# Performance work log

Measured on AMD Instinct MI355X. Metric: run time of the kernel, lower is better.

The kernel has to match this reference:

```python
import jax, jax.numpy as jnp
import numpy as np

B, S, D, H = 2, 2048, 1024, 16
HD = D // H  # head_dim = 64


def setup_inputs() -> dict:
    key = jax.random.key(0)
    ks = jax.random.split(key, 6)
    scale = 1.0 / np.sqrt(D)
    return {
        "x": jax.random.normal(ks[0], (B, S, D), dtype=jnp.float32),
        "Wq": jax.random.normal(ks[1], (D, D), dtype=jnp.float32) * scale,
        "bq": jnp.zeros((D,), dtype=jnp.float32),
        "Wk": jax.random.normal(ks[2], (D, D), dtype=jnp.float32) * scale,
        "bk": jnp.zeros((D,), dtype=jnp.float32),
        "Wv": jax.random.normal(ks[3], (D, D), dtype=jnp.float32) * scale,
        "bv": jnp.zeros((D,), dtype=jnp.float32),
        "Wo": jax.random.normal(ks[4], (D, D), dtype=jnp.float32) * scale,
        "bo": jnp.zeros((D,), dtype=jnp.float32),
    }


def reference(x, Wq, bq, Wk, bk, Wv, bv, Wo, bo):
    b, s, d = x.shape
    # q/k/v projections; torch Linear computes x @ W.T + b (W here stored as [out,in])
    q = (x @ Wq.T + bq).reshape(b, s, H, HD).transpose(0, 2, 1, 3)  # [b,h,s,hd]
    k = (x @ Wk.T + bk).reshape(b, s, H, HD).transpose(0, 2, 1, 3)
    v = (x @ Wv.T + bv).reshape(b, s, H, HD).transpose(0, 2, 1, 3)
    scores = jnp.einsum("bhqd,bhkd->bhqk", q, k) / jnp.sqrt(jnp.float32(HD))
    attn = jax.nn.softmax(scores, axis=-1)  # dropout p=0.0 -> identity
    ctx = jnp.einsum("bhqk,bhkd->bhqd", attn, v)
    ctx = ctx.transpose(0, 2, 1, 3).reshape(b, s, d)
    out = ctx @ Wo.T + bo
    return out, attn
```

## Files before the change

### kernel.cpp

```cpp
#include <hip/hip_runtime.h>
#include <hip/hip_bf16.h>


typedef __attribute__((ext_vector_type(8))) __bf16 bf16x8;
typedef __attribute__((ext_vector_type(8))) short short8;
typedef __attribute__((ext_vector_type(4))) float f32x4;
typedef __attribute__((ext_vector_type(4))) float float4v;
typedef __attribute__((ext_vector_type(4))) unsigned short ushort4v;
typedef __attribute__((ext_vector_type(8))) unsigned short ushort8v;

#define DEV static __device__ __forceinline__

DEV unsigned short f2bf(float f) {
  unsigned int u = __builtin_bit_cast(unsigned int, f);
  u += 0x7FFFu + ((u >> 16) & 1u);
  return (unsigned short)(u >> 16);
}

DEV float exp2v(float x) {
#if __has_builtin(__builtin_amdgcn_exp2f)
  return __builtin_amdgcn_exp2f(x);
#else
  return exp2f(x);
#endif
}

DEV f32x4 mfma16(short8 a, short8 b, f32x4 c) {
  return __builtin_amdgcn_mfma_f32_16x16x32_bf16(
      __builtin_bit_cast(bf16x8, a), __builtin_bit_cast(bf16x8, b), c, 0, 0, 0);
}

DEV void gld16(const void* g, void* l) {
  __builtin_amdgcn_global_load_lds(
      (const __attribute__((address_space(1))) void*)g,
      (__attribute__((address_space(3))) void*)l, 16, 0, 0);
}

#define QSCALE 0.18033688011112042f

__global__ __launch_bounds__(256) void cvt_all(
    const float* __restrict__ x, const float* __restrict__ wq,
    const float* __restrict__ wk, const float* __restrict__ wv,
    const float* __restrict__ wo, unsigned short* __restrict__ xb,
    unsigned short* __restrict__ wqb, unsigned short* __restrict__ wkb,
    unsigned short* __restrict__ wvb, unsigned short* __restrict__ wob) {
  const int bid = blockIdx.x;
  const float* s;
  unsigned short* d;
  int base;
  if (bid < 2048) {
    s = x; d = xb; base = bid * 2048;
  } else {
    const int j = bid - 2048, sel = j >> 9;
    s = sel == 0 ? wq : (sel == 1 ? wk : (sel == 2 ? wv : wo));
    d = sel == 0 ? wqb : (sel == 1 ? wkb : (sel == 2 ? wvb : wob));
    base = (j & 511) * 2048;
  }
  const int i = base + threadIdx.x * 8;
  float4v v0 = *(const float4v*)(s + i);
  float4v v1 = *(const float4v*)(s + i + 4);
  ushort8v o = {f2bf(v0[0]), f2bf(v0[1]), f2bf(v0[2]), f2bf(v0[3]),
                f2bf(v1[0]), f2bf(v1[1]), f2bf(v1[2]), f2bf(v1[3])};
  *(ushort8v*)(d + i) = o;
}

template <int WBF>
__global__ __launch_bounds__(256, 3) void gemm_qkv(
    const unsigned short* __restrict__ xb,
    const void* __restrict__ W0, const void* __restrict__ W1, const void* __restrict__ W2,
    const float* __restrict__ b0, const float* __restrict__ b1, const float* __restrict__ b2,
    unsigned short* __restrict__ Qw, unsigned short* __restrict__ Kw,
    unsigned short* __restrict__ Vt) {
  constexpr int K = 1024;
  __shared__ unsigned short As[2][128 * 32];
  __shared__ unsigned short Bs[2][128 * 32];
  const int tid = threadIdx.x, lane = tid & 63, w = tid >> 6;
  const int g = lane >> 4, ln = lane & 15;
  const int wm = (w >> 1) * 64, wn = (w & 1) * 64;
  const int work = ((int)blockIdx.x & 7) * 96 + ((int)blockIdx.x >> 3);
  const int t = work >> 8, tn = (work >> 5) & 7, tm = work & 31;
  const int m0 = tm * 128, n0 = tn * 128;
  const void* Wsel = t == 0 ? W0 : (t == 1 ? W1 : W2);
  const float* bsel = t == 0 ? b0 : (t == 1 ? b1 : b2);
  const float osc = t == 0 ? QSCALE : 1.0f;

  const unsigned short* Abase = xb + (size_t)(m0 + (tid >> 2)) * K + (tid & 3) * 8;
  const unsigned short* Bb16 = (const unsigned short*)Wsel + (size_t)(n0 + (tid >> 2)) * K + (tid & 3) * 8;
  const float* Bf32 = (const float*)Wsel + (size_t)(n0 + (tid >> 1)) * K + (tid & 1) * 16;
  const int bwoff = (tid >> 1) * 32 + (tid & 1) * 16;

  f32x4 acc[4][4] = {};

  gld16(Abase, &As[0][tid * 8]);
  gld16(Abase + (size_t)64 * K, &As[0][2048 + tid * 8]);
  if (WBF) {
    gld16(Bb16, &Bs[0][tid * 8]);
    gld16(Bb16 + (size_t)64 * K, &Bs[0][2048 + tid * 8]);
  } else {
    float4v u0 = *(const float4v*)Bf32, u1 = *(const float4v*)(Bf32 + 4);
    float4v u2 = *(const float4v*)(Bf32 + 8), u3 = *(const float4v*)(Bf32 + 12);
    ushort8v o0 = {f2bf(u0[0]), f2bf(u0[1]), f2bf(u0[2]), f2bf(u0[3]),
                   f2bf(u1[0]), f2bf(u1[1]), f2bf(u1[2]), f2bf(u1[3])};
    ushort8v o1 = {f2bf(u2[0]), f2bf(u2[1]), f2bf(u2[2]), f2bf(u2[3]),
                   f2bf(u3[0]), f2bf(u3[1]), f2bf(u3[2]), f2bf(u3[3])};
    *(ushort8v*)&Bs[0][bwoff] = o0;
    *(ushort8v*)&Bs[0][bwoff + 8] = o1;
  }

#pragma unroll 2
  for (int it = 0; it < 32; ++it) {
    __syncthreads();
    const int cur = it & 1, nxt = cur ^ 1;
    float4v u0, u1, u2, u3;
    if (it + 1 < 32) {
      const int k1 = (it + 1) * 32;
      gld16(Abase + k1, &As[nxt][tid * 8]);
      gld16(Abase + (size_t)64 * K + k1, &As[nxt][2048 + tid * 8]);
      if (WBF) {
        gld16(Bb16 + k1, &Bs[nxt][tid * 8]);
        gld16(Bb16 + (size_t)64 * K + k1, &Bs[nxt][2048 + tid * 8]);
      } else {
        u0 = *(const float4v*)(Bf32 + k1);
        u1 = *(const float4v*)(Bf32 + k1 + 4);
        u2 = *(const float4v*)(Bf32 + k1 + 8);
        u3 = *(const float4v*)(Bf32 + k1 + 12);
      }
    }
    short8 a[4], bfr[4];
#pragma unroll
    for (int fi = 0; fi < 4; ++fi)
      a[fi] = *(const short8*)&As[cur][(wm + fi * 16 + ln) * 32 + g * 8];
#pragma unroll
    for (int fj = 0; fj < 4; ++fj)
      bfr[fj] = *(const short8*)&Bs[cur][(wn + fj * 16 + ln) * 32 + g * 8];
#pragma unroll
    for (int fi = 0; fi < 4; ++fi)
#pragma unroll
      for (int fj = 0; fj < 4; ++fj) acc[fi][fj] = mfma16(a[fi], bfr[fj], acc[fi][fj]);
    if (!WBF && it + 1 < 32) {
      ushort8v o0 = {f2bf(u0[0]), f2bf(u0[1]), f2bf(u0[2]), f2bf(u0[3]),
                     f2bf(u1[0]), f2bf(u1[1]), f2bf(u1[2]), f2bf(u1[3])};
      ushort8v o1 = {f2bf(u2[0]), f2bf(u2[1]), f2bf(u2[2]), f2bf(u2[3]),
                     f2bf(u3[0]), f2bf(u3[1]), f2bf(u3[2]), f2bf(u3[3])};
      *(ushort8v*)&Bs[nxt][bwoff] = o0;
      *(ushort8v*)&Bs[nxt][bwoff + 8] = o1;
    }
  }

  if (t < 2) {
    unsigned short* Op = t == 0 ? Qw : Kw;
#pragma unroll
    for (int fi = 0; fi < 4; ++fi)
#pragma unroll
      for (int fj = 0; fj < 4; ++fj) {
        const int n = n0 + wn + fj * 16 + ln;
        const float bs = bsel[n];
#pragma unroll
        for (int rr = 0; rr < 4; ++rr) {
          const int m = m0 + wm + fi * 16 + 4 * g + rr;
          Op[(size_t)m * 1024 + n] = f2bf((acc[fi][fj][rr] + bs) * osc);
        }
      }
  } else {
    const int bb = m0 >> 11;
    const int s0 = (m0 & 2047) + wm;
#pragma unroll
    for (int fi = 0; fi < 4; ++fi)
#pragma unroll
      for (int fj = 0; fj < 4; ++fj) {
        const int n = n0 + wn + fj * 16 + ln;
        const float bs = bsel[n];
        ushort4v o = {f2bf(acc[fi][fj][0] + bs), f2bf(acc[fi][fj][1] + bs),
                      f2bf(acc[fi][fj][2] + bs), f2bf(acc[fi][fj][3] + bs)};
        *(ushort4v*)&Vt[(size_t)(bb * 1024 + n) * 2048 + s0 + fi * 16 + 4 * g] = o;
      }
  }
}

template <int WBF>
__global__ __launch_bounds__(256, 3) void gemm_o(const unsigned short* __restrict__ Cw,
                                                 const void* __restrict__ Wo,
                                                 const float* __restrict__ bo,
                                                 float* __restrict__ outp) {
  constexpr int K = 1024;
  __shared__ unsigned short As[2][128 * 32];
  __shared__ unsigned short Bs[2][128 * 32];
  const int tid = threadIdx.x, lane = tid & 63, w = tid >> 6;
  const int g = lane >> 4, ln = lane & 15;
  const int wm = (w >> 1) * 64, wn = (w & 1) * 64;
  const int work = ((int)blockIdx.x & 7) * 32 + ((int)blockIdx.x >> 3);
  const int m0 = (work & 31) * 128, n0 = (work >> 5) * 128;

  const unsigned short* Abase = Cw + (size_t)(m0 + (tid >> 2)) * K + (tid & 3) * 8;
  const unsigned short* Bb16 = (const unsigned short*)Wo + (size_t)(n0 + (tid >> 2)) * K + (tid & 3) * 8;
  const float* Bf32 = (const float*)Wo + (size_t)(n0 + (tid >> 1)) * K + (tid & 1) * 16;
  const int bwoff = (tid >> 1) * 32 + (tid & 1) * 16;

  f32x4 acc[4][4] = {};

  gld16(Abase, &As[0][tid * 8]);
  gld16(Abase + (size_t)64 * K, &As[0][2048 + tid * 8]);
  if (WBF) {
    gld16(Bb16, &Bs[0][tid * 8]);
    gld16(Bb16 + (size_t)64 * K, &Bs[0][2048 + tid * 8]);
  } else {
    float4v u0 = *(const float4v*)Bf32, u1 = *(const float4v*)(Bf32 + 4);
    float4v u2 = *(const float4v*)(Bf32 + 8), u3 = *(const float4v*)(Bf32 + 12);
    ushort8v o0 = {f2bf(u0[0]), f2bf(u0[1]), f2bf(u0[2]), f2bf(u0[3]),
                   f2bf(u1[0]), f2bf(u1[1]), f2bf(u1[2]), f2bf(u1[3])};
    ushort8v o1 = {f2bf(u2[0]), f2bf(u2[1]), f2bf(u2[2]), f2bf(u2[3]),
                   f2bf(u3[0]), f2bf(u3[1]), f2bf(u3[2]), f2bf(u3[3])};
    *(ushort8v*)&Bs[0][bwoff] = o0;
    *(ushort8v*)&Bs[0][bwoff + 8] = o1;
  }

#pragma unroll 2
  for (int it = 0; it < 32; ++it) {
    __syncthreads();
    const int cur = it & 1, nxt = cur ^ 1;
    float4v u0, u1, u2, u3;
    if (it + 1 < 32) {
      const int k1 = (it + 1) * 32;
      gld16(Abase + k1, &As[nxt][tid * 8]);
      gld16(Abase + (size_t)64 * K + k1, &As[nxt][2048 + tid * 8]);
      if (WBF) {
        gld16(Bb16 + k1, &Bs[nxt][tid * 8]);
        gld16(Bb16 + (size_t)64 * K + k1, &Bs[nxt][2048 + tid * 8]);
      } else {
        u0 = *(const float4v*)(Bf32 + k1);
        u1 = *(const float4v*)(Bf32 + k1 + 4);
        u2 = *(const float4v*)(Bf32 + k1 + 8);
        u3 = *(const float4v*)(Bf32 + k1 + 12);
      }
    }
    short8 a[4], bfr[4];
#pragma unroll
    for (int fi = 0; fi < 4; ++fi)
      a[fi] = *(const short8*)&As[cur][(wm + fi * 16 + ln) * 32 + g * 8];
#pragma unroll
    for (int fj = 0; fj < 4; ++fj)
      bfr[fj] = *(const short8*)&Bs[cur][(wn + fj * 16 + ln) * 32 + g * 8];
#pragma unroll
    for (int fi = 0; fi < 4; ++fi)
#pragma unroll
      for (int fj = 0; fj < 4; ++fj) acc[fi][fj] = mfma16(a[fi], bfr[fj], acc[fi][fj]);
    if (!WBF && it + 1 < 32) {
      ushort8v o0 = {f2bf(u0[0]), f2bf(u0[1]), f2bf(u0[2]), f2bf(u0[3]),
                     f2bf(u1[0]), f2bf(u1[1]), f2bf(u1[2]), f2bf(u1[3])};
      ushort8v o1 = {f2bf(u2[0]), f2bf(u2[1]), f2bf(u2[2]), f2bf(u2[3]),
                     f2bf(u3[0]), f2bf(u3[1]), f2bf(u3[2]), f2bf(u3[3])};
      *(ushort8v*)&Bs[nxt][bwoff] = o0;
      *(ushort8v*)&Bs[nxt][bwoff + 8] = o1;
    }
  }

#pragma unroll
  for (int fi = 0; fi < 4; ++fi)
#pragma unroll
    for (int fj = 0; fj < 4; ++fj) {
      const int n = n0 + wn + fj * 16 + ln;
      const float bs = bo[n];
#pragma unroll
      for (int rr = 0; rr < 4; ++rr) {
        const int m = m0 + wm + fi * 16 + 4 * g + rr;
        outp[(size_t)m * 1024 + n] = acc[fi][fj][rr] + bs;
      }
    }
}

__global__ __launch_bounds__(512, 4) void attn_kernel(
    const unsigned short* __restrict__ Qg, const unsigned short* __restrict__ Kg,
    const unsigned short* __restrict__ Vt, float* __restrict__ attn_out,
    unsigned short* __restrict__ ctx) {
  constexpr int LDP = 72;
  __shared__ unsigned short Ps[128 * LDP];
  __shared__ unsigned short Ks[2][64 * 64];
  __shared__ unsigned short Vs[2][64 * 64];
  const int tid = threadIdx.x, lane = tid & 63, w = tid >> 6;
  const int g = lane >> 4, ln = lane & 15;
  const int work = ((int)blockIdx.x & 7) * 64 + ((int)blockIdx.x >> 3);
  const int qt = work & 15, h = (work >> 4) & 15, b = work >> 8;
  const int q0 = qt * 128;
  const size_t kbase = (size_t)b * 2048 * 1024 + (size_t)h * 64;
  const size_t vbase = ((size_t)b * 1024 + h * 64) * 2048;

  short8 qf[2];
#pragma unroll
  for (int hh = 0; hh < 2; ++hh)
    qf[hh] = *(const short8*)(Qg + kbase + (size_t)(q0 + w * 16 + ln) * 1024 +
                              hh * 32 + 8 * g);

  const int sr = tid >> 3, sb = tid & 7;
  const int swz = ((sb ^ (sr & 7)) * 8);
  const unsigned short* Ksrc = Kg + kbase + (size_t)sr * 1024 + swz;
  const unsigned short* Vsrc = Vt + vbase + (size_t)sr * 2048 + swz;

  float lp = 0.f;
  gld16(Ksrc, &Ks[0][tid * 8]);
#pragma unroll 2
  for (int kc = 0; kc < 32; ++kc) {
    __syncthreads();
    if (kc + 1 < 32)
      gld16(Ksrc + (size_t)(kc + 1) * 64 * 1024, &Ks[(kc + 1) & 1][tid * 8]);
    const unsigned short* Kc = Ks[kc & 1];
#pragma unroll
    for (int fk = 0; fk < 4; ++fk) {
      const int row = fk * 16 + ln;
      const short8 kf0 = *(const short8*)&Kc[row * 64 + ((g ^ (ln & 7)) * 8)];
      const short8 kf1 = *(const short8*)&Kc[row * 64 + (((4 + g) ^ (ln & 7)) * 8)];
      f32x4 z = {0.f, 0.f, 0.f, 0.f};
      __builtin_amdgcn_s_setprio(1);
      z = mfma16(kf0, qf[0], z);
      z = mfma16(kf1, qf[1], z);
      __builtin_amdgcn_s_setprio(0);
      lp += exp2v(z[0]) + exp2v(z[1]) + exp2v(z[2]) + exp2v(z[3]);
    }
  }
  lp += __shfl_xor(lp, 16);
  lp += __shfl_xor(lp, 32);
  const float lb = -log2f(lp);

  __syncthreads();
  gld16(Ksrc, &Ks[0][tid * 8]);
  gld16(Vsrc, &Vs[0][tid * 8]);
  f32x4 c_[4] = {};
  const size_t attnbase = ((size_t)(b * 16 + h) * 2048 + q0 + w * 16) * 2048;
#pragma unroll 2
  for (int kc = 0; kc < 32; ++kc) {
    __syncthreads();
    if (kc + 1 < 32) {
      gld16(Ksrc + (size_t)(kc + 1) * 64 * 1024, &Ks[(kc + 1) & 1][tid * 8]);
      gld16(Vsrc + (kc + 1) * 64, &Vs[(kc + 1) & 1][tid * 8]);
    }
    const unsigned short* Kc = Ks[kc & 1];
    const unsigned short* Vc = Vs[kc & 1];
#pragma unroll
    for (int fk = 0; fk < 4; ++fk) {
      const int row = fk * 16 + ln;
      const short8 kf0 = *(const short8*)&Kc[row * 64 + ((g ^ (ln & 7)) * 8)];
      const short8 kf1 = *(const short8*)&Kc[row * 64 + (((4 + g) ^ (ln & 7)) * 8)];
      f32x4 z = {lb, lb, lb, lb};
      __builtin_amdgcn_s_setprio(1);
      z = mfma16(kf0, qf[0], z);
      z = mfma16(kf1, qf[1], z);
      __builtin_amdgcn_s_setprio(0);
      float4v pv = {exp2v(z[0]), exp2v(z[1]), exp2v(z[2]), exp2v(z[3])};
      *(float4v*)&attn_out[attnbase + (size_t)ln * 2048 + kc * 64 + fk * 16 + 4 * g] = pv;
      ushort4v pb = {f2bf(pv[0]), f2bf(pv[1]), f2bf(pv[2]), f2bf(pv[3])};
      *(ushort4v*)&Ps[(w * 16 + ln) * LDP + fk * 16 + 4 * g] = pb;
    }
#pragma unroll
    for (int ks = 0; ks < 2; ++ks) {
      const short8 pa = *(const short8*)&Ps[(w * 16 + ln) * LDP + ks * 32 + 8 * g];
      __builtin_amdgcn_s_setprio(1);
#pragma unroll
      for (int fd = 0; fd < 4; ++fd) {
        const int d = fd * 16 + ln;
        const short8 vb = *(const short8*)&Vc[d * 64 + (((ks * 4 + g) ^ (ln & 7)) * 8)];
        c_[fd] = mfma16(pa, vb, c_[fd]);
      }
      __builtin_amdgcn_s_setprio(0);
    }
  }

#pragma unroll
  for (int fd = 0; fd < 4; ++fd)
#pragma unroll
    for (int rr = 0; rr < 4; ++rr) {
      const int q = w * 16 + 4 * g + rr;
      ctx[(size_t)(b * 2048 + q0 + q) * 1024 + h * 64 + fd * 16 + ln] = f2bf(c_[fd][rr]);
    }
}

extern "C" void kernel_launch(void* const* d_in, const int* in_sizes, int n_in,
                              void* d_out, int out_size, void* d_ws, size_t ws_size,
                              hipStream_t stream) {
  const float* x  = (const float*)d_in[0];
  const float* Wq = (const float*)d_in[1];
  const float* bq = (const float*)d_in[2];
  const float* Wk = (const float*)d_in[3];
  const float* bk = (const float*)d_in[4];
  const float* Wv = (const float*)d_in[5];
  const float* bv = (const float*)d_in[6];
  const float* Wo = (const float*)d_in[7];
  const float* bo = (const float*)d_in[8];

  float* outp = (float*)d_out;
  float* attnp = outp + (size_t)4194304;

  unsigned short* Qw = (unsigned short*)d_ws;
  unsigned short* Kw = Qw + (size_t)4194304;
  unsigned short* Vt = Kw + (size_t)4194304;
  unsigned short* Cw = Vt + (size_t)4194304;

  const bool wbf = ws_size >= (size_t)40 * 1024 * 1024;
  dim3 blk(256, 1, 1);

  if (wbf) {
    unsigned short* Wqb = Cw + (size_t)4194304;
    unsigned short* Wkb = Wqb + (size_t)1048576;
    unsigned short* Wvb = Wkb + (size_t)1048576;
    unsigned short* Wob = Wvb + (size_t)1048576;
    cvt_all<<<dim3(4096), blk, 0, stream>>>(x, Wq, Wk, Wv, Wo, Cw, Wqb, Wkb, Wvb, Wob);
    gemm_qkv<1><<<dim3(768), blk, 0, stream>>>(Cw, Wqb, Wkb, Wvb, bq, bk, bv, Qw, Kw, Vt);
    attn_kernel<<<dim3(512), dim3(512), 0, stream>>>(Qw, Kw, Vt, attnp, Cw);
    gemm_o<1><<<dim3(256), blk, 0, stream>>>(Cw, Wob, bo, outp);
  } else {
    cvt_all<<<dim3(2048), blk, 0, stream>>>(x, Wq, Wk, Wv, Wo, Cw, nullptr, nullptr,
                                            nullptr, nullptr);
    gemm_qkv<0><<<dim3(768), blk, 0, stream>>>(Cw, Wq, Wk, Wv, bq, bk, bv, Qw, Kw, Vt);
    attn_kernel<<<dim3(512), dim3(512), 0, stream>>>(Qw, Kw, Vt, attnp, Cw);
    gemm_o<0><<<dim3(256), blk, 0, stream>>>(Cw, Wo, bo, outp);
  }
}
```

Baseline: 245.1 us.

## Triple-buffer K/V tiles in attention with prefetch distance two and explicit vmcnt waits

```diff
diff --git a/kernel.cpp b/kernel.cpp
--- a/kernel.cpp
+++ b/kernel.cpp
@@ -274,8 +274,8 @@
     unsigned short* __restrict__ ctx) {
   constexpr int LDP = 72;
   __shared__ unsigned short Ps[128 * LDP];
-  __shared__ unsigned short Ks[2][64 * 64];
-  __shared__ unsigned short Vs[2][64 * 64];
+  __shared__ unsigned short Ks[3][64 * 64];
+  __shared__ unsigned short Vs[3][64 * 64];
   const int tid = threadIdx.x, lane = tid & 63, w = tid >> 6;
   const int g = lane >> 4, ln = lane & 15;
   const int work = ((int)blockIdx.x & 7) * 64 + ((int)blockIdx.x >> 3);
@@ -297,12 +297,18 @@
 
   float lp = 0.f;
   gld16(Ksrc, &Ks[0][tid * 8]);
-#pragma unroll 2
+  gld16(Ksrc + (size_t)64 * 1024, &Ks[1][tid * 8]);
   for (int kc = 0; kc < 32; ++kc) {
-    __syncthreads();
-    if (kc + 1 < 32)
-      gld16(Ksrc + (size_t)(kc + 1) * 64 * 1024, &Ks[(kc + 1) & 1][tid * 8]);
-    const unsigned short* Kc = Ks[kc & 1];
+    if (kc < 31)
+      asm volatile("s_waitcnt vmcnt(1)" ::: "memory");
+    else
+      asm volatile("s_waitcnt vmcnt(0)" ::: "memory");
+    __builtin_amdgcn_s_barrier();
+    __builtin_amdgcn_sched_barrier(0);
+    if (kc + 2 < 32)
+      gld16(Ksrc + (size_t)(kc + 2) * 64 * 1024, &Ks[(kc + 2) % 3][tid * 8]);
+    __builtin_amdgcn_sched_barrier(0);
+    const unsigned short* Kc = Ks[kc % 3];
 #pragma unroll
     for (int fk = 0; fk < 4; ++fk) {
       const int row = fk * 16 + ln;
@@ -321,19 +327,29 @@
   const float lb = -log2f(lp);
 
   __syncthreads();
+
   gld16(Ksrc, &Ks[0][tid * 8]);
   gld16(Vsrc, &Vs[0][tid * 8]);
+  gld16(Ksrc + (size_t)64 * 1024, &Ks[1][tid * 8]);
+  gld16(Vsrc + 64, &Vs[1][tid * 8]);
   f32x4 c_[4] = {};
   const size_t attnbase = ((size_t)(b * 16 + h) * 2048 + q0 + w * 16) * 2048;
-#pragma unroll 2
   for (int kc = 0; kc < 32; ++kc) {
-    __syncthreads();
-    if (kc + 1 < 32) {
-      gld16(Ksrc + (size_t)(kc + 1) * 64 * 1024, &Ks[(kc + 1) & 1][tid * 8]);
-      gld16(Vsrc + (kc + 1) * 64, &Vs[(kc + 1) & 1][tid * 8]);
-    }
-    const unsigned short* Kc = Ks[kc & 1];
-    const unsigned short* Vc = Vs[kc & 1];
+    if (kc == 0)
+      asm volatile("s_waitcnt vmcnt(2)" ::: "memory");
+    else if (kc == 1)
+      asm volatile("s_waitcnt vmcnt(6)" ::: "memory");
+    else
+      asm volatile("s_waitcnt vmcnt(8)" ::: "memory");
+    __builtin_amdgcn_s_barrier();
+    __builtin_amdgcn_sched_barrier(0);
+    if (kc + 2 < 32) {
+      gld16(Ksrc + (size_t)(kc + 2) * 64 * 1024, &Ks[(kc + 2) % 3][tid * 8]);
+      gld16(Vsrc + (kc + 2) * 64, &Vs[(kc + 2) % 3][tid * 8]);
+    }
+    __builtin_amdgcn_sched_barrier(0);
+    const unsigned short* Kc = Ks[kc % 3];
+    const unsigned short* Vc = Vs[kc % 3];
 #pragma unroll
     for (int fk = 0; fk < 4; ++fk) {
       const int row = fk * 16 + ln;
```

New measurement: 244.8 us. Within noise of the previous version (-0.1%).

## Split attention row-sum pass into separate kernel parallelised over key halves

Applied to the files above, without the earlier changes.

```diff
diff --git a/kernel.cpp b/kernel.cpp
--- a/kernel.cpp
+++ b/kernel.cpp
@@ -268,10 +268,60 @@
     }
 }
 
-__global__ __launch_bounds__(512, 4) void attn_kernel(
+__global__ __launch_bounds__(512, 6) void attn_pass1(
     const unsigned short* __restrict__ Qg, const unsigned short* __restrict__ Kg,
-    const unsigned short* __restrict__ Vt, float* __restrict__ attn_out,
-    unsigned short* __restrict__ ctx) {
+    float* __restrict__ lpart) {
+  __shared__ unsigned short Ks[2][64 * 64];
+  const int tid = threadIdx.x, lane = tid & 63, w = tid >> 6;
+  const int g = lane >> 4, ln = lane & 15;
+  const int work = ((int)blockIdx.x & 7) * 128 + ((int)blockIdx.x >> 3);
+  const int qt = work & 15, h = (work >> 4) & 15, b = (work >> 8) & 1, kh = work >> 9;
+  const int q0 = qt * 128;
+  const size_t kbase = (size_t)b * 2048 * 1024 + (size_t)h * 64;
+
+  short8 qf[2];
+#pragma unroll
+  for (int hh = 0; hh < 2; ++hh)
+    qf[hh] = *(const short8*)(Qg + kbase + (size_t)(q0 + w * 16 + ln) * 1024 +
+                              hh * 32 + 8 * g);
+
+  const int sr = tid >> 3, sb = tid & 7;
+  const int swz = ((sb ^ (sr & 7)) * 8);
+  const unsigned short* Ksrc = Kg + kbase + (size_t)(kh * 1024 + sr) * 1024 + swz;
+
+  float lp = 0.f;
+  gld16(Ksrc, &Ks[0][tid * 8]);
+#pragma unroll 2
+  for (int kc = 0; kc < 16; ++kc) {
+    __syncthreads();
+    if (kc + 1 < 16)
+      gld16(Ksrc + (size_t)(kc + 1) * 64 * 1024, &Ks[(kc + 1) & 1][tid * 8]);
+    const unsigned short* Kc = Ks[kc & 1];
+#pragma unroll
+    for (int fk = 0; fk < 4; ++fk) {
+      const int row = fk * 16 + ln;
+      const short8 kf0 = *(const short8*)&Kc[row * 64 + ((g ^ (ln & 7)) * 8)];
+      const short8 kf1 = *(const short8*)&Kc[row * 64 + (((4 + g) ^ (ln & 7)) * 8)];
+      f32x4 z = {0.f, 0.f, 0.f, 0.f};
+      __builtin_amdgcn_s_setprio(1);
+      z = mfma16(kf0, qf[0], z);
+      z = mfma16(kf1, qf[1], z);
+      __builtin_amdgcn_s_setprio(0);
+      lp += exp2v(z[0]) + exp2v(z[1]) + exp2v(z[2]) + exp2v(z[3]);
+    }
+  }
+  lp += __shfl_xor(lp, 16);
+  lp += __shfl_xor(lp, 32);
+  if (g == 0 && lane < 16) {
+    const size_t q = (size_t)(b * 16 + h) * 2048 + q0 + w * 16 + ln;
+    lpart[(q << 1) + kh] = lp;
+  }
+}
+
+__global__ __launch_bounds__(512, 4) void attn_pass2(
+    const unsigned short* __restrict__ Qg, const unsigned short* __restrict__ Kg,
+    const unsigned short* __restrict__ Vt, const float* __restrict__ lpart,
+    float* __restrict__ attn_out, unsigned short* __restrict__ ctx) {
   constexpr int LDP = 72;
   __shared__ unsigned short Ps[128 * LDP];
   __shared__ unsigned short Ks[2][64 * 64];
@@ -290,37 +340,14 @@
     qf[hh] = *(const short8*)(Qg + kbase + (size_t)(q0 + w * 16 + ln) * 1024 +
                               hh * 32 + 8 * g);
 
+  const size_t qidx = (size_t)(b * 16 + h) * 2048 + q0 + w * 16 + ln;
+  const float lb = -log2f(lpart[qidx << 1] + lpart[(qidx << 1) + 1]);
+
   const int sr = tid >> 3, sb = tid & 7;
   const int swz = ((sb ^ (sr & 7)) * 8);
   const unsigned short* Ksrc = Kg + kbase + (size_t)sr * 1024 + swz;
   const unsigned short* Vsrc = Vt + vbase + (size_t)sr * 2048 + swz;
 
-  float lp = 0.f;
-  gld16(Ksrc, &Ks[0][tid * 8]);
-#pragma unroll 2
-  for (int kc = 0; kc < 32; ++kc) {
-    __syncthreads();
-    if (kc + 1 < 32)
-      gld16(Ksrc + (size_t)(kc + 1) * 64 * 1024, &Ks[(kc + 1) & 1][tid * 8]);
-    const unsigned short* Kc = Ks[kc & 1];
-#pragma unroll
-    for (int fk = 0; fk < 4; ++fk) {
-      const int row = fk * 16 + ln;
-      const short8 kf0 = *(const short8*)&Kc[row * 64 + ((g ^ (ln & 7)) * 8)];
-      const short8 kf1 = *(const short8*)&Kc[row * 64 + (((4 + g) ^ (ln & 7)) * 8)];
-      f32x4 z = {0.f, 0.f, 0.f, 0.f};
-      __builtin_amdgcn_s_setprio(1);
-      z = mfma16(kf0, qf[0], z);
-      z = mfma16(kf1, qf[1], z);
-      __builtin_amdgcn_s_setprio(0);
-      lp += exp2v(z[0]) + exp2v(z[1]) + exp2v(z[2]) + exp2v(z[3]);
-    }
-  }
-  lp += __shfl_xor(lp, 16);
-  lp += __shfl_xor(lp, 32);
-  const float lb = -log2f(lp);
-
-  __syncthreads();
   gld16(Ksrc, &Ks[0][tid * 8]);
   gld16(Vsrc, &Vs[0][tid * 8]);
   f32x4 c_[4] = {};
@@ -393,7 +420,7 @@
   unsigned short* Vt = Kw + (size_t)4194304;
   unsigned short* Cw = Vt + (size_t)4194304;
 
-  const bool wbf = ws_size >= (size_t)40 * 1024 * 1024;
+  const bool wbf = ws_size >= (size_t)41 * 1024 * 1024;
   dim3 blk(256, 1, 1);
 
   if (wbf) {
@@ -401,15 +428,19 @@
     unsigned short* Wkb = Wqb + (size_t)1048576;
     unsigned short* Wvb = Wkb + (size_t)1048576;
     unsigned short* Wob = Wvb + (size_t)1048576;
+    float* lpart = (float*)(Wob + (size_t)1048576);
     cvt_all<<<dim3(4096), blk, 0, stream>>>(x, Wq, Wk, Wv, Wo, Cw, Wqb, Wkb, Wvb, Wob);
     gemm_qkv<1><<<dim3(768), blk, 0, stream>>>(Cw, Wqb, Wkb, Wvb, bq, bk, bv, Qw, Kw, Vt);
-    attn_kernel<<<dim3(512), dim3(512), 0, stream>>>(Qw, Kw, Vt, attnp, Cw);
+    attn_pass1<<<dim3(1024), dim3(512), 0, stream>>>(Qw, Kw, lpart);
+    attn_pass2<<<dim3(512), dim3(512), 0, stream>>>(Qw, Kw, Vt, lpart, attnp, Cw);
     gemm_o<1><<<dim3(256), blk, 0, stream>>>(Cw, Wob, bo, outp);
   } else {
+    float* lpart = (float*)(Cw + (size_t)4194304);
     cvt_all<<<dim3(2048), blk, 0, stream>>>(x, Wq, Wk, Wv, Wo, Cw, nullptr, nullptr,
                                             nullptr, nullptr);
     gemm_qkv<0><<<dim3(768), blk, 0, stream>>>(Cw, Wq, Wk, Wv, bq, bk, bv, Qw, Kw, Vt);
-    attn_kernel<<<dim3(512), dim3(512), 0, stream>>>(Qw, Kw, Vt, attnp, Cw);
+    attn_pass1<<<dim3(1024), dim3(512), 0, stream>>>(Qw, Kw, lpart);
+    attn_pass2<<<dim3(512), dim3(512), 0, stream>>>(Qw, Kw, Vt, lpart, attnp, Cw);
     gemm_o<0><<<dim3(256), blk, 0, stream>>>(Cw, Wo, bo, outp);
   }
 }
```

Result: slower. 254.5 us (+3.8%).

## Load K/V fragments directly from global memory instead of LDS staging

Applied to the files above, without the earlier changes.

```diff
diff --git a/kernel.cpp b/kernel.cpp
--- a/kernel.cpp
+++ b/kernel.cpp
@@ -268,14 +268,12 @@
     }
 }
 
-__global__ __launch_bounds__(512, 4) void attn_kernel(
+__global__ __launch_bounds__(512) void attn_kernel(
     const unsigned short* __restrict__ Qg, const unsigned short* __restrict__ Kg,
     const unsigned short* __restrict__ Vt, float* __restrict__ attn_out,
     unsigned short* __restrict__ ctx) {
   constexpr int LDP = 72;
   __shared__ unsigned short Ps[128 * LDP];
-  __shared__ unsigned short Ks[2][64 * 64];
-  __shared__ unsigned short Vs[2][64 * 64];
   const int tid = threadIdx.x, lane = tid & 63, w = tid >> 6;
   const int g = lane >> 4, ln = lane & 15;
   const int work = ((int)blockIdx.x & 7) * 64 + ((int)blockIdx.x >> 3);
@@ -290,24 +288,16 @@
     qf[hh] = *(const short8*)(Qg + kbase + (size_t)(q0 + w * 16 + ln) * 1024 +
                               hh * 32 + 8 * g);
 
-  const int sr = tid >> 3, sb = tid & 7;
-  const int swz = ((sb ^ (sr & 7)) * 8);
-  const unsigned short* Ksrc = Kg + kbase + (size_t)sr * 1024 + swz;
-  const unsigned short* Vsrc = Vt + vbase + (size_t)sr * 2048 + swz;
+  const unsigned short* Kf = Kg + kbase + (size_t)ln * 1024 + 8 * g;
+  const unsigned short* Vf = Vt + vbase + (size_t)ln * 2048 + 16 * g;
 
   float lp = 0.f;
-  gld16(Ksrc, &Ks[0][tid * 8]);
-#pragma unroll 2
   for (int kc = 0; kc < 32; ++kc) {
-    __syncthreads();
-    if (kc + 1 < 32)
-      gld16(Ksrc + (size_t)(kc + 1) * 64 * 1024, &Ks[(kc + 1) & 1][tid * 8]);
-    const unsigned short* Kc = Ks[kc & 1];
 #pragma unroll
     for (int fk = 0; fk < 4; ++fk) {
-      const int row = fk * 16 + ln;
-      const short8 kf0 = *(const short8*)&Kc[row * 64 + ((g ^ (ln & 7)) * 8)];
-      const short8 kf1 = *(const short8*)&Kc[row * 64 + (((4 + g) ^ (ln & 7)) * 8)];
+      const unsigned short* kp = Kf + (size_t)(kc * 64 + fk * 16) * 1024;
+      const short8 kf0 = *(const short8*)kp;
+      const short8 kf1 = *(const short8*)(kp + 32);
       f32x4 z = {0.f, 0.f, 0.f, 0.f};
       __builtin_amdgcn_s_setprio(1);
       z = mfma16(kf0, qf[0], z);
@@ -320,25 +310,14 @@
   lp += __shfl_xor(lp, 32);
   const float lb = -log2f(lp);
 
-  __syncthreads();
-  gld16(Ksrc, &Ks[0][tid * 8]);
-  gld16(Vsrc, &Vs[0][tid * 8]);
   f32x4 c_[4] = {};
   const size_t attnbase = ((size_t)(b * 16 + h) * 2048 + q0 + w * 16) * 2048;
-#pragma unroll 2
   for (int kc = 0; kc < 32; ++kc) {
-    __syncthreads();
-    if (kc + 1 < 32) {
-      gld16(Ksrc + (size_t)(kc + 1) * 64 * 1024, &Ks[(kc + 1) & 1][tid * 8]);
-      gld16(Vsrc + (kc + 1) * 64, &Vs[(kc + 1) & 1][tid * 8]);
-    }
-    const unsigned short* Kc = Ks[kc & 1];
-    const unsigned short* Vc = Vs[kc & 1];
 #pragma unroll
     for (int fk = 0; fk < 4; ++fk) {
-      const int row = fk * 16 + ln;
-      const short8 kf0 = *(const short8*)&Kc[row * 64 + ((g ^ (ln & 7)) * 8)];
-      const short8 kf1 = *(const short8*)&Kc[row * 64 + (((4 + g) ^ (ln & 7)) * 8)];
+      const unsigned short* kp = Kf + (size_t)(kc * 64 + fk * 16) * 1024;
+      const short8 kf0 = *(const short8*)kp;
+      const short8 kf1 = *(const short8*)(kp + 32);
       f32x4 z = {lb, lb, lb, lb};
       __builtin_amdgcn_s_setprio(1);
       z = mfma16(kf0, qf[0], z);
@@ -355,8 +334,8 @@
       __builtin_amdgcn_s_setprio(1);
 #pragma unroll
       for (int fd = 0; fd < 4; ++fd) {
-        const int d = fd * 16 + ln;
-        const short8 vb = *(const short8*)&Vc[d * 64 + (((ks * 4 + g) ^ (ln & 7)) * 8)];
+        const short8 vb =
+            *(const short8*)(Vf + (size_t)(fd * 16) * 2048 + kc * 64 + ks * 32 - 8 * g);
         c_[fd] = mfma16(pa, vb, c_[fd]);
       }
       __builtin_amdgcn_s_setprio(0);
```

Result: slower. 511.1 us (+108.5%).
